# Optimization experiments

Hardware: AMD Instinct MI355X
Metric: run time of the kernel (lower is better)

The kernel has to match this reference:

```python
import jax, jax.numpy as jnp
import numpy as np


def setup_inputs() -> dict:
    key = jax.random.key(0)
    k1, k2, k3, k4 = jax.random.split(key, 4)
    B, Cin, Cout, N, modes = 16, 128, 128, 8192, 64
    scale = 1.0 / (Cin * Cout)
    x = jax.random.normal(k1, (B, Cin, N), dtype=jnp.float32)
    # spectral weight: [in, out, modes, 2] uniform in [0, scale) like torch.rand * scale
    w_spec = scale * jax.random.uniform(k2, (Cin, Cout, modes, 2), dtype=jnp.float32)
    # Conv1d(kernel=1) weight [out, in] and bias [out] (kaiming-uniform-ish init)
    bound = 1.0 / np.sqrt(Cin)
    w_conv = jax.random.uniform(k3, (Cout, Cin), minval=-bound, maxval=bound, dtype=jnp.float32)
    b_conv = jax.random.uniform(k4, (Cout,), minval=-bound, maxval=bound, dtype=jnp.float32)
    return {"x": x, "w_spec": w_spec, "w_conv": w_conv, "b_conv": b_conv}


def reference(x, w_spec, w_conv, b_conv):
    N = x.shape[-1]
    modes = w_spec.shape[2]
    n_freq = N // 2 + 1
    # Spectral conv: rfft, keep first `modes` coefficients, complex channel mix
    x_ft = jnp.fft.rfft(x)  # [B, Cin, n_freq] complex64
    w_c = w_spec[..., 0] + 1j * w_spec[..., 1]  # [Cin, Cout, modes]
    out_m = jnp.einsum('bim,iom->bom', x_ft[:, :, :modes], w_c)  # [B, Cout, modes]
    out_ft = jnp.pad(out_m, ((0, 0), (0, 0), (0, n_freq - modes)))
    x1 = jnp.fft.irfft(out_ft, n=N)  # [B, Cout, N]
    # 1x1 conv (pointwise channel mix)
    x2 = jnp.einsum('bin,oi->bon', x, w_conv) + b_conv[None, :, None]
    return jax.nn.gelu(x1 + x2, approximate=False)
```

## Files before the change

### kernel.cpp

```cpp
#include <hip/hip_runtime.h>
#include <hip/hip_bf16.h>
#include <math.h>

#define NB    16
#define NCIN  128
#define NCOUT 128
#define NN    8192
#define NMOD  64

typedef short bf16x8 __attribute__((ext_vector_type(8)));
typedef float f32x4  __attribute__((ext_vector_type(4)));

#define MFMA16(a, b, c) __builtin_amdgcn_mfma_f32_16x16x32_bf16((a), (b), (c), 0, 0, 0)

__device__ inline unsigned short f2bf_rne(float f) {
    unsigned u = __float_as_uint(f);
    u += 0x7FFF + ((u >> 16) & 1);
    return (unsigned short)(u >> 16);
}
__device__ inline short f2bf_trunc(float f) {
    return (short)(__float_as_uint(f) >> 16);
}

__global__ __launch_bounds__(256) void k_prep(const float* __restrict__ wc,
                                              unsigned short* __restrict__ T,
                                              unsigned short* __restrict__ Tt,
                                              unsigned short* __restrict__ Wcb) {
    const float C = 7.66990393943e-4f;
    if (blockIdx.x < 16) {
        int a = blockIdx.x * 256 + threadIdx.x;
        int k = a >> 6, n0 = (a & 63) * 128;
        for (int j8 = 0; j8 < 16; ++j8) {
            short c8[8], s8[8];
            #pragma unroll
            for (int j = 0; j < 8; ++j) {
                int n = n0 + j8 * 8 + j;
                int ph = (k * n) & (NN - 1);
                float sn, cs; __sincosf((float)ph * C, &sn, &cs);
                c8[j] = (short)f2bf_rne(cs);
                s8[j] = (short)f2bf_rne(-sn);
            }
            *(bf16x8*)(T + (size_t)(2 * k) * NN + n0 + j8 * 8)     = *(bf16x8*)c8;
            *(bf16x8*)(T + (size_t)(2 * k + 1) * NN + n0 + j8 * 8) = *(bf16x8*)s8;
        }
    } else if (blockIdx.x < 48) {
        int n = (blockIdx.x - 16) * 256 + threadIdx.x;
        for (int k4 = 0; k4 < 16; ++k4) {
            short buf[8];
            #pragma unroll
            for (int j = 0; j < 4; ++j) {
                int k = k4 * 4 + j;
                int ph = (n * k) & (NN - 1);
                float sn, cs; __sincosf((float)ph * C, &sn, &cs);
                buf[2 * j]     = (short)f2bf_rne(cs);
                buf[2 * j + 1] = (short)f2bf_rne(-sn);
            }
            *(bf16x8*)(Tt + (size_t)n * 128 + k4 * 8) = *(bf16x8*)buf;
        }
    } else {
        int j = (blockIdx.x - 48) * 256 + threadIdx.x;
        if (j < NCOUT * NCIN) Wcb[j] = f2bf_rne(wc[j]);
    }
}

__global__ __launch_bounds__(256) void k_dftmm(const float* __restrict__ x,
                                               const unsigned short* __restrict__ T,
                                               float* __restrict__ Cpart) {
    const int mt = blockIdx.x & 31, sp = blockIdx.x >> 5;
    const int w = threadIdx.x >> 6, l = threadIdx.x & 63;
    const int l15 = l & 15, q = l >> 4;
    const int colbase = w * 32;
    f32x4 acc[4][2] = {};
    for (int kt = 0; kt < 16; ++kt) {
        const int kb = sp * 512 + kt * 32;
        bf16x8 a[4], bb[2];
        #pragma unroll
        for (int mf = 0; mf < 4; ++mf) {
            const float* ap = x + (size_t)(mt * 64 + mf * 16 + l15) * NN + kb + q * 8;
            float4 f0 = *(const float4*)ap;
            float4 f1 = *(const float4*)(ap + 4);
            short t8[8] = { f2bf_trunc(f0.x), f2bf_trunc(f0.y), f2bf_trunc(f0.z), f2bf_trunc(f0.w),
                            f2bf_trunc(f1.x), f2bf_trunc(f1.y), f2bf_trunc(f1.z), f2bf_trunc(f1.w) };
            a[mf] = *(bf16x8*)t8;
        }
        #pragma unroll
        for (int nf = 0; nf < 2; ++nf)
            bb[nf] = *(const bf16x8*)(T + (size_t)(colbase + nf * 16 + l15) * NN + kb + q * 8);
        #pragma unroll
        for (int mf = 0; mf < 4; ++mf) {
            acc[mf][0] = MFMA16(a[mf], bb[0], acc[mf][0]);
            acc[mf][1] = MFMA16(a[mf], bb[1], acc[mf][1]);
        }
    }
    #pragma unroll
    for (int mf = 0; mf < 4; ++mf)
        #pragma unroll
        for (int nf = 0; nf < 2; ++nf)
            #pragma unroll
            for (int r = 0; r < 4; ++r) {
                int row = mt * 64 + mf * 16 + q * 4 + r;
                int col = colbase + nf * 16 + l15;
                Cpart[((size_t)sp * 2048 + row) * 128 + col] = acc[mf][nf][r];
            }
}

__global__ __launch_bounds__(256) void k_reduce(const float* __restrict__ Cpart,
                                                float* __restrict__ Xf) {
    int t = blockIdx.x * 256 + threadIdx.x;
    float s = 0.f;
    #pragma unroll
    for (int sp = 0; sp < 16; ++sp) s += Cpart[(size_t)sp * 262144 + t];
    Xf[t] = s;
}

__global__ __launch_bounds__(256) void k_mix(const float* __restrict__ Xf,
                                             const float* __restrict__ wsp,
                                             unsigned short* __restrict__ Aspec) {
    int t = blockIdx.x * 256 + threadIdx.x;
    int k = t & 63, o = (t >> 6) & 127, b = t >> 13;
    const float* xf = Xf + (size_t)b * (NCIN * 128) + k * 2;
    const float* w  = wsp + (size_t)o * 128 + k * 2;
    float sr = 0.f, si = 0.f;
    #pragma unroll 4
    for (int i = 0; i < NCIN; ++i) {
        float xr = xf[i * 128], xi = xf[i * 128 + 1];
        float wr = w[(size_t)i * 16384], wi = w[(size_t)i * 16384 + 1];
        sr += xr * wr - xi * wi;
        si += xr * wi + xi * wr;
    }
    if (k == 0) { sr *= (1.f / NN); si = 0.f; }
    else        { sr *= (2.f / NN); si *= (2.f / NN); }
    unsigned short pair[2] = { f2bf_rne(sr), f2bf_rne(si) };
    *(unsigned int*)(Aspec + ((size_t)(b * 128 + o)) * 128 + 2 * k) = *(unsigned int*)pair;
}

__global__ __launch_bounds__(256) void k_out(const float* __restrict__ x,
                                             const unsigned short* __restrict__ Tt,
                                             const unsigned short* __restrict__ Aspec,
                                             const unsigned short* __restrict__ Wcb,
                                             const float* __restrict__ bias,
                                             float* __restrict__ out) {
    const int b = blockIdx.x >> 6, nt = blockIdx.x & 63;
    const int w = threadIdx.x >> 6, l = threadIdx.x & 63;
    const int l15 = l & 15, q = l >> 4;
    const int nbase = nt * 128 + w * 32;
    f32x4 acc[8][2] = {};
    for (int kt = 0; kt < 8; ++kt) {
        bf16x8 bb[2];
        if (kt < 4) {
            #pragma unroll
            for (int nf = 0; nf < 2; ++nf) {
                int n = nbase + nf * 16 + l15;
                bb[nf] = *(const bf16x8*)(Tt + (size_t)n * 128 + kt * 32 + q * 8);
            }
        } else {
            int i0 = (kt - 4) * 32 + q * 8;
            #pragma unroll
            for (int nf = 0; nf < 2; ++nf) {
                int n = nbase + nf * 16 + l15;
                const float* xp = x + ((size_t)(b * 128 + i0)) * NN + n;
                short t8[8];
                #pragma unroll
                for (int j = 0; j < 8; ++j) t8[j] = f2bf_trunc(xp[(size_t)j * NN]);
                bb[nf] = *(bf16x8*)t8;
            }
        }
        const unsigned short* Ap = (kt < 4)
            ? (Aspec + (size_t)b * 128 * 128 + kt * 32 + q * 8)
            : (Wcb + (kt - 4) * 32 + q * 8);
        #pragma unroll
        for (int mf = 0; mf < 8; ++mf) {
            bf16x8 a = *(const bf16x8*)(Ap + (size_t)(mf * 16 + l15) * 128);
            acc[mf][0] = MFMA16(a, bb[0], acc[mf][0]);
            acc[mf][1] = MFMA16(a, bb[1], acc[mf][1]);
        }
    }
    #pragma unroll
    for (int mf = 0; mf < 8; ++mf)
        #pragma unroll
        for (int nf = 0; nf < 2; ++nf)
            #pragma unroll
            for (int r = 0; r < 4; ++r) {
                int o = mf * 16 + q * 4 + r;
                int n = nbase + nf * 16 + l15;
                float v = acc[mf][nf][r] + bias[o];
                float u = v * v;
                float p = v * fmaf(0.0713548162f, u, 1.5957691216f);
                float e = __expf(-p);
                float g = v * __builtin_amdgcn_rcpf(1.f + e);
                out[((size_t)(b * 128 + o)) * NN + n] = g;
            }
}

extern "C" void kernel_launch(void* const* d_in, const int* in_sizes, int n_in,
                              void* d_out, int out_size, void* d_ws, size_t ws_size,
                              hipStream_t stream) {
    const float* x    = (const float*)d_in[0];
    const float* wsp  = (const float*)d_in[1];
    const float* wc   = (const float*)d_in[2];
    const float* bc   = (const float*)d_in[3];
    float* out = (float*)d_out;

    unsigned short* T   = (unsigned short*)d_ws;
    unsigned short* Tt  = T + (size_t)1048576;
    unsigned short* Wcb = Tt + (size_t)1048576;
    unsigned short* Asp = Wcb + 16384;
    float* Cpart = (float*)(Asp + 262144);
    float* Xf    = Cpart + (size_t)16 * 262144;

    k_prep  <<<112,  256, 0, stream>>>(wc, T, Tt, Wcb);
    k_dftmm <<<512,  256, 0, stream>>>(x, T, Cpart);
    k_reduce<<<1024, 256, 0, stream>>>(Cpart, Xf);
    k_mix   <<<512,  256, 0, stream>>>(Xf, wsp, Asp);
    k_out   <<<1024, 256, 0, stream>>>(x, Tt, Asp, Wcb, bc, out);
}
```

Before: 224.7 us.

## Run spectral channel mix on MFMA and stage x through swizzled LDS

The scalar complex channel-mix kernel becomes an MFMA kernel. k_prep now also packs the spectral weights into bf16 real/imaginary blocks with the normalisation folded in, and the DFT partial results are written column-major so each mode's batch-by-channel slice is contiguous. k_out loads its x tile once into XOR-swizzled shared memory with coalesced float4 reads, replacing strided per-element global gathers for the pointwise-conv GEMM. The costs are bf16 rounding of the spectral products, a larger workspace, the weight repacking done on every call, and 32KB of LDS per block, which can lower occupancy.

```diff
diff --git a/kernel.cpp b/kernel.cpp
--- a/kernel.cpp
+++ b/kernel.cpp
@@ -23,9 +23,11 @@
 }
 
 __global__ __launch_bounds__(256) void k_prep(const float* __restrict__ wc,
+                                              const float* __restrict__ wsp,
                                               unsigned short* __restrict__ T,
                                               unsigned short* __restrict__ Tt,
-                                              unsigned short* __restrict__ Wcb) {
+                                              unsigned short* __restrict__ Wcb,
+                                              unsigned short* __restrict__ Wpk) {
     const float C = 7.66990393943e-4f;
     if (blockIdx.x < 16) {
         int a = blockIdx.x * 256 + threadIdx.x;
@@ -57,9 +59,33 @@
             }
             *(bf16x8*)(Tt + (size_t)n * 128 + k4 * 8) = *(bf16x8*)buf;
         }
-    } else {
+    } else if (blockIdx.x < 112) {
         int j = (blockIdx.x - 48) * 256 + threadIdx.x;
         if (j < NCOUT * NCIN) Wcb[j] = f2bf_rne(wc[j]);
+    } else {
+        int g2 = (blockIdx.x - 112) * 256 + threadIdx.x;
+        int k  = g2 & 63;
+        int o  = (g2 >> 6) & 127;
+        int ch = g2 >> 13;
+        const float s = (k == 0) ? (1.f / NN) : (2.f / NN);
+        const float2* wp = (const float2*)wsp;
+        unsigned short* wre = Wpk + ((size_t)(k * 2 + 0) * 128 + o) * 256;
+        unsigned short* wim = Wpk + ((size_t)(k * 2 + 1) * 128 + o) * 256;
+        for (int c = ch * 8; c < ch * 8 + 8; ++c) {
+            int i0 = 4 * c;
+            short re8[8], im8[8];
+            #pragma unroll
+            for (int t2 = 0; t2 < 4; ++t2) {
+                float2 wv = wp[((size_t)(i0 + t2) * 128 + o) * 64 + k];
+                float wr = s * wv.x, wi = s * wv.y;
+                re8[2 * t2]     = (short)f2bf_rne(wr);
+                re8[2 * t2 + 1] = (short)f2bf_rne(-wi);
+                im8[2 * t2]     = (k == 0) ? (short)0 : (short)f2bf_rne(wi);
+                im8[2 * t2 + 1] = (k == 0) ? (short)0 : (short)f2bf_rne(wr);
+            }
+            *(bf16x8*)(wre + c * 8) = *(bf16x8*)re8;
+            *(bf16x8*)(wim + c * 8) = *(bf16x8*)im8;
+        }
     }
 }
 
@@ -95,13 +121,11 @@
     #pragma unroll
     for (int mf = 0; mf < 4; ++mf)
         #pragma unroll
-        for (int nf = 0; nf < 2; ++nf)
-            #pragma unroll
-            for (int r = 0; r < 4; ++r) {
-                int row = mt * 64 + mf * 16 + q * 4 + r;
-                int col = colbase + nf * 16 + l15;
-                Cpart[((size_t)sp * 2048 + row) * 128 + col] = acc[mf][nf][r];
-            }
+        for (int nf = 0; nf < 2; ++nf) {
+            int col  = colbase + nf * 16 + l15;
+            int row0 = mt * 64 + mf * 16 + q * 4;
+            *(f32x4*)(Cpart + (size_t)sp * 262144 + (size_t)col * 2048 + row0) = acc[mf][nf];
+        }
 }
 
 __global__ __launch_bounds__(256) void k_reduce(const float* __restrict__ Cpart,
@@ -113,25 +137,44 @@
     Xf[t] = s;
 }
 
-__global__ __launch_bounds__(256) void k_mix(const float* __restrict__ Xf,
-                                             const float* __restrict__ wsp,
-                                             unsigned short* __restrict__ Aspec) {
-    int t = blockIdx.x * 256 + threadIdx.x;
-    int k = t & 63, o = (t >> 6) & 127, b = t >> 13;
-    const float* xf = Xf + (size_t)b * (NCIN * 128) + k * 2;
-    const float* w  = wsp + (size_t)o * 128 + k * 2;
-    float sr = 0.f, si = 0.f;
-    #pragma unroll 4
-    for (int i = 0; i < NCIN; ++i) {
-        float xr = xf[i * 128], xi = xf[i * 128 + 1];
-        float wr = w[(size_t)i * 16384], wi = w[(size_t)i * 16384 + 1];
-        sr += xr * wr - xi * wi;
-        si += xr * wi + xi * wr;
-    }
-    if (k == 0) { sr *= (1.f / NN); si = 0.f; }
-    else        { sr *= (2.f / NN); si *= (2.f / NN); }
-    unsigned short pair[2] = { f2bf_rne(sr), f2bf_rne(si) };
-    *(unsigned int*)(Aspec + ((size_t)(b * 128 + o)) * 128 + 2 * k) = *(unsigned int*)pair;
+__global__ __launch_bounds__(64) void k_mixmm(const float* __restrict__ Xf,
+                                              const unsigned short* __restrict__ Wpk,
+                                              unsigned short* __restrict__ Aspec) {
+    const int k = blockIdx.x >> 2, oq = blockIdx.x & 3;
+    const int l = threadIdx.x, l15 = l & 15, q = l >> 4;
+    f32x4 ar[2] = {}, ai[2] = {};
+    const float* xr = Xf + (size_t)(2 * k) * 2048 + l15 * 128;
+    const float* xi = xr + 2048;
+    #pragma unroll
+    for (int kt = 0; kt < 8; ++kt) {
+        int i0 = kt * 16 + q * 4;
+        float4 r4 = *(const float4*)(xr + i0);
+        float4 i4 = *(const float4*)(xi + i0);
+        short a8[8] = { (short)f2bf_rne(r4.x), (short)f2bf_rne(i4.x),
+                        (short)f2bf_rne(r4.y), (short)f2bf_rne(i4.y),
+                        (short)f2bf_rne(r4.z), (short)f2bf_rne(i4.z),
+                        (short)f2bf_rne(r4.w), (short)f2bf_rne(i4.w) };
+        bf16x8 a = *(bf16x8*)a8;
+        #pragma unroll
+        for (int nf = 0; nf < 2; ++nf) {
+            int o = oq * 32 + nf * 16 + l15;
+            const unsigned short* wb = Wpk + ((size_t)(k * 2) * 128 + o) * 256 + kt * 32 + q * 8;
+            bf16x8 bre = *(const bf16x8*)wb;
+            bf16x8 bim = *(const bf16x8*)(wb + 32768);
+            ar[nf] = MFMA16(a, bre, ar[nf]);
+            ai[nf] = MFMA16(a, bim, ai[nf]);
+        }
+    }
+    #pragma unroll
+    for (int nf = 0; nf < 2; ++nf) {
+        int o = oq * 32 + nf * 16 + l15;
+        #pragma unroll
+        for (int r = 0; r < 4; ++r) {
+            int b = q * 4 + r;
+            unsigned v = (unsigned)f2bf_rne(ar[nf][r]) | ((unsigned)f2bf_rne(ai[nf][r]) << 16);
+            *(unsigned*)(Aspec + ((size_t)b * 128 + o) * 128 + 2 * k) = v;
+        }
+    }
 }
 
 __global__ __launch_bounds__(256) void k_out(const float* __restrict__ x,
@@ -143,31 +186,39 @@
     const int b = blockIdx.x >> 6, nt = blockIdx.x & 63;
     const int w = threadIdx.x >> 6, l = threadIdx.x & 63;
     const int l15 = l & 15, q = l >> 4;
-    const int nbase = nt * 128 + w * 32;
+    __shared__ short xs[16384];
+
+    const float* xb = x + (size_t)b * 128 * NN + nt * 128;
+    #pragma unroll
+    for (int it = 0; it < 8; ++it) {
+        int unit = it * 256 + threadIdx.x;
+        int ipair = unit >> 5, nq = unit & 31;
+        int i0 = ipair * 2;
+        const float* p0 = xb + (size_t)i0 * NN + nq * 4;
+        float4 r0 = *(const float4*)p0;
+        float4 r1 = *(const float4*)(p0 + NN);
+        float a0[4] = { r0.x, r0.y, r0.z, r0.w };
+        float a1[4] = { r1.x, r1.y, r1.z, r1.w };
+        #pragma unroll
+        for (int j = 0; j < 4; ++j) {
+            int n = nq * 4 + j;
+            unsigned v = (unsigned)(unsigned short)f2bf_trunc(a0[j])
+                       | ((unsigned)(unsigned short)f2bf_trunc(a1[j]) << 16);
+            int addr = n * 128 + (((i0 >> 3) ^ (n & 15)) * 8) + (i0 & 7);
+            *(unsigned*)&xs[addr] = v;
+        }
+    }
+
     f32x4 acc[8][2] = {};
-    for (int kt = 0; kt < 8; ++kt) {
+    #pragma unroll
+    for (int kt = 0; kt < 4; ++kt) {
         bf16x8 bb[2];
-        if (kt < 4) {
-            #pragma unroll
-            for (int nf = 0; nf < 2; ++nf) {
-                int n = nbase + nf * 16 + l15;
-                bb[nf] = *(const bf16x8*)(Tt + (size_t)n * 128 + kt * 32 + q * 8);
-            }
-        } else {
-            int i0 = (kt - 4) * 32 + q * 8;
-            #pragma unroll
-            for (int nf = 0; nf < 2; ++nf) {
-                int n = nbase + nf * 16 + l15;
-                const float* xp = x + ((size_t)(b * 128 + i0)) * NN + n;
-                short t8[8];
-                #pragma unroll
-                for (int j = 0; j < 8; ++j) t8[j] = f2bf_trunc(xp[(size_t)j * NN]);
-                bb[nf] = *(bf16x8*)t8;
-            }
-        }
-        const unsigned short* Ap = (kt < 4)
-            ? (Aspec + (size_t)b * 128 * 128 + kt * 32 + q * 8)
-            : (Wcb + (kt - 4) * 32 + q * 8);
+        #pragma unroll
+        for (int nf = 0; nf < 2; ++nf) {
+            int n = nt * 128 + w * 32 + nf * 16 + l15;
+            bb[nf] = *(const bf16x8*)(Tt + (size_t)n * 128 + kt * 32 + q * 8);
+        }
+        const unsigned short* Ap = Aspec + (size_t)b * 16384 + kt * 32 + q * 8;
         #pragma unroll
         for (int mf = 0; mf < 8; ++mf) {
             bf16x8 a = *(const bf16x8*)(Ap + (size_t)(mf * 16 + l15) * 128);
@@ -175,6 +226,24 @@
             acc[mf][1] = MFMA16(a, bb[1], acc[mf][1]);
         }
     }
+    __syncthreads();
+    #pragma unroll
+    for (int kt = 0; kt < 4; ++kt) {
+        bf16x8 bb[2];
+        #pragma unroll
+        for (int nf = 0; nf < 2; ++nf) {
+            int nl = w * 32 + nf * 16 + l15;
+            int c  = kt * 4 + q;
+            bb[nf] = *(const bf16x8*)&xs[nl * 128 + ((c ^ (nl & 15)) * 8)];
+        }
+        const unsigned short* Ap = Wcb + kt * 32 + q * 8;
+        #pragma unroll
+        for (int mf = 0; mf < 8; ++mf) {
+            bf16x8 a = *(const bf16x8*)(Ap + (size_t)(mf * 16 + l15) * 128);
+            acc[mf][0] = MFMA16(a, bb[0], acc[mf][0]);
+            acc[mf][1] = MFMA16(a, bb[1], acc[mf][1]);
+        }
+    }
     #pragma unroll
     for (int mf = 0; mf < 8; ++mf)
         #pragma unroll
@@ -182,7 +251,7 @@
             #pragma unroll
             for (int r = 0; r < 4; ++r) {
                 int o = mf * 16 + q * 4 + r;
-                int n = nbase + nf * 16 + l15;
+                int n = nt * 128 + w * 32 + nf * 16 + l15;
                 float v = acc[mf][nf][r] + bias[o];
                 float u = v * v;
                 float p = v * fmaf(0.0713548162f, u, 1.5957691216f);
@@ -205,12 +274,13 @@
     unsigned short* Tt  = T + (size_t)1048576;
     unsigned short* Wcb = Tt + (size_t)1048576;
     unsigned short* Asp = Wcb + 16384;
-    float* Cpart = (float*)(Asp + 262144);
+    unsigned short* Wpk = Asp + 262144;
+    float* Cpart = (float*)(Wpk + (size_t)8388608);
     float* Xf    = Cpart + (size_t)16 * 262144;
 
-    k_prep  <<<112,  256, 0, stream>>>(wc, T, Tt, Wcb);
+    k_prep  <<<240,  256, 0, stream>>>(wc, wsp, T, Tt, Wcb, Wpk);
     k_dftmm <<<512,  256, 0, stream>>>(x, T, Cpart);
     k_reduce<<<1024, 256, 0, stream>>>(Cpart, Xf);
-    k_mix   <<<512,  256, 0, stream>>>(Xf, wsp, Asp);
+    k_mixmm <<<256,  64,  0, stream>>>(Xf, Wpk, Asp);
     k_out   <<<1024, 256, 0, stream>>>(x, Tt, Asp, Wcb, bc, out);
 }
```

Result: no change. 221.3 us (-1.5%).
